# Performance work log

Measured on AMD Instinct MI355X. Metric: run time of the kernel, lower is better.

Reference implementation:

```python
import jax, jax.numpy as jnp
import numpy as np

N = 4096      # tokens
D = 4096      # input_dim
O = 4096      # output_dim
E = 8         # n_experts
R = 16        # LoRA rank (same for all experts)
K = 2         # top_k
TEMP = 1.0    # temperature
ALPHA = 1.0   # LoRA alpha


def setup_inputs() -> dict:
    key = jax.random.key(0)
    ks = jax.random.split(key, 7)
    std = 1.0 / np.sqrt(R)  # LoRALayer init: randn(input_dim, rank) * 1/sqrt(rank)
    return {
        "x": jax.random.normal(ks[0], (N, D), jnp.float32),
        "linear_w": jax.random.normal(ks[1], (D, O), jnp.float32) * 0.02,  # base nn.Linear weight (stored [in,out])
        "linear_b": jnp.zeros((O,), jnp.float32),
        "lora_A": jax.random.normal(ks[2], (E, D, R), jnp.float32) * std,
        "lora_B": jax.random.normal(ks[3], (E, R, O), jnp.float32) * 0.02,  # torch inits B to 0; randomized for nontrivial test
        "gate_w": jax.random.normal(ks[4], (E + 1, D), jnp.float32) * 0.02,  # E+1 GateLayers, each [D,1]
        "bvv": jax.random.randint(ks[5], (N, E), 0, 2, jnp.int32),  # basis_variant_binary_vector (unused in static gating)
    }


def reference(x, linear_w, linear_b, lora_A, lora_B, gate_w, bvv):
    # base path: nn.Linear
    base = x @ linear_w + linear_b                                   # [N, O]
    # all experts evaluated densely: alpha * (x @ A_e @ B_e), batched as grouped GEMMs
    lora = ALPHA * jnp.einsum("ner,ero->neo",
                              jnp.einsum("nd,edr->ner", x, lora_A),
                              lora_B)                                # [N, E, O]
    outputs = jnp.concatenate([base[:, None, :], lora], axis=1)      # [N, E+1, O]

    # static top-k gating
    logits = x @ gate_w.T                                            # [N, E+1]
    base_logits, lora_logits = logits[:, :1], logits[:, 1:]
    top_vals, top_idx = jax.lax.top_k(lora_logits, K)                # [N, K]
    rows = jnp.arange(x.shape[0])[:, None]
    # torch: zeros.scatter(top_idx, top_vals) -> non-selected experts keep logit 0.0
    lora_sparse = jnp.zeros_like(lora_logits).at[rows, top_idx].set(top_vals)
    gates = jax.nn.softmax(
        jnp.concatenate([base_logits, lora_sparse], axis=-1) / TEMP, axis=-1
    )                                                                # [N, E+1]

    return jnp.sum(outputs * gates[..., None], axis=1)               # [N, O]
```

## Files before the change

kernel.cpp:

```cpp
#include <hip/hip_runtime.h>
#include <hip/hip_bf16.h>
#include <math.h>

constexpr int Ncfg = 4096;
constexpr int Dcfg = 4096;
constexpr int Ocfg = 4096;
constexpr int Ecfg = 8;
constexpr int Rcfg = 16;
constexpr int KD   = Dcfg + Ecfg * Rcfg;
constexpr float ALPHA_C = 1.0f;
constexpr double TEMP_C = 1.0;

constexpr size_t BT_OFF = 0;
constexpr size_t AP_OFF = BT_OFF + (size_t)Ocfg * KD * 2;
constexpr size_t AT_OFF = AP_OFF + (size_t)Ncfg * KD * 2;
constexpr size_t G_OFF  = AT_OFF + (size_t)Ecfg * Rcfg * Dcfg * 2;

typedef short bf16x8 __attribute__((ext_vector_type(8)));
typedef float f32x4  __attribute__((ext_vector_type(4)));

__device__ __forceinline__ void async_load16(const __hip_bfloat16* g, __hip_bfloat16* l) {
  __builtin_amdgcn_global_load_lds((__attribute__((address_space(1))) void*)(g),
                                   (__attribute__((address_space(3))) void*)(l), 16, 0, 0);
}

__global__ __launch_bounds__(256) void prep_parallel_kernel(
    const float* __restrict__ x,  const float* __restrict__ gw,
    const float* __restrict__ W,  const float* __restrict__ lB,
    const float* __restrict__ lA,
    float* __restrict__ gates, __hip_bfloat16* __restrict__ Ap,
    __hip_bfloat16* __restrict__ BT, __hip_bfloat16* __restrict__ AT) {
  __shared__ union {
    float tile[64][65];
    float atile[256][17];
  } sm;
  const int bid = blockIdx.x;
  const int tid = threadIdx.x;

  if (bid < 512) {
    const int wave = tid >> 6, lane = tid & 63;
    const int na = bid * 8 + wave * 2, nb = na + 1;
    const float4* xa4 = (const float4*)(x + (size_t)na * Dcfg);
    const float4* xb4 = (const float4*)(x + (size_t)nb * Dcfg);
    const float4* gw4 = (const float4*)gw;
    double accA[9], accB[9];
#pragma unroll
    for (int e = 0; e < 9; e++) { accA[e] = 0.0; accB[e] = 0.0; }
    for (int i = 0; i < 16; i++) {
      int fi = lane + 64 * i;
      float4 xa = xa4[fi], xb = xb4[fi];
#pragma unroll
      for (int e = 0; e < 9; e++) {
        float4 w = gw4[e * 1024 + fi];
        accA[e] += (double)xa.x * (double)w.x + (double)xa.y * (double)w.y +
                   (double)xa.z * (double)w.z + (double)xa.w * (double)w.w;
        accB[e] += (double)xb.x * (double)w.x + (double)xb.y * (double)w.y +
                   (double)xb.z * (double)w.z + (double)xb.w * (double)w.w;
      }
    }
#pragma unroll
    for (int off = 32; off >= 1; off >>= 1) {
#pragma unroll
      for (int e = 0; e < 9; e++) {
        accA[e] += __shfl_xor(accA[e], off, 64);
        accB[e] += __shfl_xor(accB[e], off, 64);
      }
    }
    float g0A_l = 0.f, g0B_l = 0.f;
    if (lane == 0) {
#pragma unroll
      for (int r = 0; r < 2; r++) {
        double lg[9];
#pragma unroll
        for (int e = 0; e < 9; e++) lg[e] = r ? accB[e] : accA[e];
        int i1 = 1;
        for (int e = 2; e <= 8; e++) if (lg[e] > lg[i1]) i1 = e;
        int i2 = -1; double v2 = -1e300;
        for (int e = 1; e <= 8; e++) if (e != i1 && lg[e] > v2) { v2 = lg[e]; i2 = e; }
        double vals[9];
        vals[0] = lg[0];
        for (int e = 1; e <= 8; e++) vals[e] = (e == i1 || e == i2) ? lg[e] : 0.0;
        double mx = vals[0];
        for (int e = 1; e < 9; e++) mx = fmax(mx, vals[e]);
        double se = 0.0, ex[9];
        for (int e = 0; e < 9; e++) { ex[e] = exp((vals[e] - mx) / TEMP_C); se += ex[e]; }
        const int n = r ? nb : na;
        for (int e = 0; e < 9; e++) gates[n * 16 + e] = (float)(ex[e] / se);
        if (r == 0) g0A_l = (float)(ex[0] / se); else g0B_l = (float)(ex[0] / se);
      }
    }
    const float g0A = __shfl(g0A_l, 0, 64);
    const float g0B = __shfl(g0B_l, 0, 64);
    __hip_bfloat16* ara = Ap + (size_t)na * KD;
    __hip_bfloat16* arb = Ap + (size_t)nb * KD;
    for (int i = 0; i < 16; i++) {
      int fi = lane + 64 * i;
      float4 xa = xa4[fi], xb = xb4[fi];
      union { ushort4 u; __hip_bfloat16 h[4]; } p;
      p.h[0] = __float2bfloat16(g0A * xa.x);
      p.h[1] = __float2bfloat16(g0A * xa.y);
      p.h[2] = __float2bfloat16(g0A * xa.z);
      p.h[3] = __float2bfloat16(g0A * xa.w);
      *(ushort4*)(ara + (size_t)fi * 4) = p.u;
      p.h[0] = __float2bfloat16(g0B * xb.x);
      p.h[1] = __float2bfloat16(g0B * xb.y);
      p.h[2] = __float2bfloat16(g0B * xb.z);
      p.h[3] = __float2bfloat16(g0B * xb.w);
      *(ushort4*)(arb + (size_t)fi * 4) = p.u;
    }
  } else if (bid < 4736) {
    const float* src; int r0, c0, dstOff;
    if (bid < 4608) {
      int id = bid - 512;
      src = W; r0 = (id & 63) * 64; c0 = (id >> 6) * 64; dstOff = 0;
    } else {
      int id = bid - 4608;
      src = lB; r0 = (id & 1) * 64; c0 = (id >> 1) * 64; dstOff = Dcfg;
    }
#pragma unroll
    for (int it = 0; it < 4; it++) {
      int flat = it * 256 + tid;
      int i = flat >> 4, f = flat & 15;
      float4 v = *(const float4*)(src + (size_t)(r0 + i) * Ocfg + c0 + 4 * f);
      sm.tile[i][4 * f + 0] = v.x;
      sm.tile[i][4 * f + 1] = v.y;
      sm.tile[i][4 * f + 2] = v.z;
      sm.tile[i][4 * f + 3] = v.w;
    }
    __syncthreads();
#pragma unroll
    for (int it = 0; it < 4; it++) {
      int flat = it * 256 + tid;
      int j = flat >> 4, q = flat & 15;
      union { ushort4 u; __hip_bfloat16 h[4]; } p;
      p.h[0] = __float2bfloat16(sm.tile[4 * q + 0][j]);
      p.h[1] = __float2bfloat16(sm.tile[4 * q + 1][j]);
      p.h[2] = __float2bfloat16(sm.tile[4 * q + 2][j]);
      p.h[3] = __float2bfloat16(sm.tile[4 * q + 3][j]);
      *(ushort4*)(BT + (size_t)(c0 + j) * KD + dstOff + r0 + 4 * q) = p.u;
    }
  } else {
    const int id = bid - 4736;
    const int e = id >> 4, d0 = (id & 15) * 256;
#pragma unroll
    for (int it = 0; it < 16; it++) {
      int idx = it * 256 + tid;
      int d = idx >> 4, rr = idx & 15;
      sm.atile[d][rr] = lA[((size_t)e * Dcfg + d0 + d) * Rcfg + rr];
    }
    __syncthreads();
#pragma unroll
    for (int rr = 0; rr < Rcfg; rr++) {
      AT[((size_t)e * Rcfg + rr) * Dcfg + d0 + tid] = __float2bfloat16(sm.atile[tid][rr]);
    }
  }
}

__global__ __launch_bounds__(512) void lora_t_kernel(
    const float* __restrict__ x, const __hip_bfloat16* __restrict__ AT,
    const float* __restrict__ gates, __hip_bfloat16* __restrict__ Ap) {
  const int n0 = blockIdx.x * 16;
  const int tid = threadIdx.x;
  const int wave = tid >> 6, lane = tid & 63;
  const int m = lane & 15, quad = lane >> 4;
  const int kbase = wave * 512;

  f32x4 acc[8] = {};
  const float* xrow = x + (size_t)(n0 + m) * Dcfg + kbase + quad * 8;
  const __hip_bfloat16* atb = AT + (size_t)m * Dcfg + kbase + quad * 8;
#pragma unroll 2
  for (int kb = 0; kb < 512; kb += 32) {
    float4 x0 = *(const float4*)(xrow + kb);
    float4 x1 = *(const float4*)(xrow + kb + 4);
    union { bf16x8 v; __hip_bfloat16 h[8]; } a;
    a.h[0] = __float2bfloat16(x0.x); a.h[1] = __float2bfloat16(x0.y);
    a.h[2] = __float2bfloat16(x0.z); a.h[3] = __float2bfloat16(x0.w);
    a.h[4] = __float2bfloat16(x1.x); a.h[5] = __float2bfloat16(x1.y);
    a.h[6] = __float2bfloat16(x1.z); a.h[7] = __float2bfloat16(x1.w);
#pragma unroll
    for (int e = 0; e < Ecfg; e++) {
      bf16x8 b = *(const bf16x8*)(atb + (size_t)e * Rcfg * Dcfg + kb);
      acc[e] = __builtin_amdgcn_mfma_f32_16x16x32_bf16(a.v, b, acc[e], 0, 0, 0);
    }
  }
  __shared__ f32x4 red[8][8][64];
#pragma unroll
  for (int e = 0; e < Ecfg; e++) red[wave][e][lane] = acc[e];
  __syncthreads();
  {
    const int e = wave;
    f32x4 s = red[0][e][lane];
#pragma unroll
    for (int w = 1; w < 8; w++) s += red[w][e][lane];
#pragma unroll
    for (int rg = 0; rg < 4; rg++) {
      int nn = n0 + quad * 4 + rg;
      float g = gates[nn * 16 + 1 + e];
      Ap[(size_t)nn * KD + Dcfg + e * Rcfg + m] = __float2bfloat16(ALPHA_C * g * s[rg]);
    }
  }
}

__global__ __launch_bounds__(256) void gemm_kernel(
    const __hip_bfloat16* __restrict__ Ap, const __hip_bfloat16* __restrict__ BT,
    const float* __restrict__ gates, const float* __restrict__ bias,
    float* __restrict__ out) {
  __shared__ __hip_bfloat16 As[128 * 32];
  __shared__ __hip_bfloat16 Bs[128 * 32];
  const int tid = threadIdx.x;
  const int m0 = blockIdx.y * 128, n0 = blockIdx.x * 128;
  const int wave = tid >> 6, lane = tid & 63;
  const int wm = (wave & 1) * 64, wn = (wave >> 1) * 64;
  const int mr = lane & 15, quad = lane >> 4;

  f32x4 acc[4][4] = {};

  const int srow = tid >> 2;
  const int kc = (tid & 3) * 8;
  const __hip_bfloat16* gA0 = Ap + (size_t)(m0 + srow) * KD + kc;
  const __hip_bfloat16* gA1 = gA0 + (size_t)64 * KD;
  const __hip_bfloat16* gB0 = BT + (size_t)(n0 + srow) * KD + kc;
  const __hip_bfloat16* gB1 = gB0 + (size_t)64 * KD;
  __hip_bfloat16* lA0 = As + tid * 8;
  __hip_bfloat16* lA1 = As + 64 * 32 + tid * 8;
  __hip_bfloat16* lB0 = Bs + tid * 8;
  __hip_bfloat16* lB1 = Bs + 64 * 32 + tid * 8;

  for (int kb = 0; kb < KD; kb += 32) {
    __syncthreads();
    async_load16(gA0 + kb, lA0);
    async_load16(gA1 + kb, lA1);
    async_load16(gB0 + kb, lB0);
    async_load16(gB1 + kb, lB1);
    asm volatile("s_waitcnt vmcnt(0)" ::: "memory");
    __syncthreads();

    bf16x8 a[4], b[4];
#pragma unroll
    for (int i = 0; i < 4; i++)
      a[i] = *(const bf16x8*)&As[(wm + i * 16 + mr) * 32 + quad * 8];
#pragma unroll
    for (int j = 0; j < 4; j++)
      b[j] = *(const bf16x8*)&Bs[(wn + j * 16 + mr) * 32 + quad * 8];
#pragma unroll
    for (int i = 0; i < 4; i++)
#pragma unroll
      for (int j = 0; j < 4; j++)
        acc[i][j] = __builtin_amdgcn_mfma_f32_16x16x32_bf16(a[i], b[j], acc[i][j], 0, 0, 0);
  }

#pragma unroll
  for (int i = 0; i < 4; i++) {
    const int rowb = m0 + wm + i * 16 + quad * 4;
#pragma unroll
    for (int rg = 0; rg < 4; rg++) {
      const int row = rowb + rg;
      const float g0 = gates[row * 16];
#pragma unroll
      for (int j = 0; j < 4; j++) {
        const int col = n0 + wn + j * 16 + mr;
        out[(size_t)row * Ocfg + col] = acc[i][j][rg] + g0 * bias[col];
      }
    }
  }
}

extern "C" void kernel_launch(void* const* d_in, const int* in_sizes, int n_in,
                              void* d_out, int out_size, void* d_ws, size_t ws_size,
                              hipStream_t stream) {
  const float* x  = (const float*)d_in[0];
  const float* W  = (const float*)d_in[1];
  const float* b  = (const float*)d_in[2];
  const float* lA = (const float*)d_in[3];
  const float* lB = (const float*)d_in[4];
  const float* gw = (const float*)d_in[5];
  float* out = (float*)d_out;

  char* ws = (char*)d_ws;
  __hip_bfloat16* BT    = (__hip_bfloat16*)(ws + BT_OFF);
  __hip_bfloat16* Ap    = (__hip_bfloat16*)(ws + AP_OFF);
  __hip_bfloat16* AT    = (__hip_bfloat16*)(ws + AT_OFF);
  float*          gates = (float*)(ws + G_OFF);

  prep_parallel_kernel<<<dim3(4864), 256, 0, stream>>>(x, gw, W, lB, lA, gates, Ap, BT, AT);
  lora_t_kernel<<<dim3(Ncfg / 16), 512, 0, stream>>>(x, AT, gates, Ap);
  gemm_kernel<<<dim3(Ocfg / 128, Ncfg / 128), 256, 0, stream>>>(Ap, BT, gates, b, out);
}
```

Before: 400.9 us.

## Rewrite GEMM with 256x256 tiles, double-buffered async LDS loads, and swizzling

Replaces the 128x128 single-buffered GEMM with a 256x256 tile, 512-thread kernel that double-buffers K=64 tiles in 128KB of LDS, loading the next tile while MFMAs run, and XOR-swizzles the LDS layout to avoid bank conflicts. The work is split into four MFMA phases interleaved with barriers and s_setprio. This targets the load-then-wait stall in the old loop and raises data reuse per tile. The larger tile gives only 256 blocks, so CU occupancy and load balance may suffer, and the large LDS footprint limits resident blocks.

```diff
diff --git a/kernel.cpp b/kernel.cpp
--- a/kernel.cpp
+++ b/kernel.cpp
@@ -8,6 +8,7 @@
 constexpr int Ecfg = 8;
 constexpr int Rcfg = 16;
 constexpr int KD   = Dcfg + Ecfg * Rcfg;
+constexpr int NKT  = KD / 64;
 constexpr float ALPHA_C = 1.0f;
 constexpr double TEMP_C = 1.0;
 
@@ -201,66 +202,152 @@
   }
 }
 
-__global__ __launch_bounds__(256) void gemm_kernel(
+#define STG(gbase, lbase, u, ktile)                                              \
+  __builtin_amdgcn_global_load_lds(                                              \
+      (__attribute__((address_space(1))) void*)((gbase) + (size_t)(u) * 64 * KD  \
+                                                + (size_t)(ktile) * 64),         \
+      (__attribute__((address_space(3))) void*)((lbase) + (u) * 8192 + dst),     \
+      16, 0, 0)
+
+__global__ __launch_bounds__(512, 2) void gemm_kernel(
     const __hip_bfloat16* __restrict__ Ap, const __hip_bfloat16* __restrict__ BT,
     const float* __restrict__ gates, const float* __restrict__ bias,
     float* __restrict__ out) {
-  __shared__ __hip_bfloat16 As[128 * 32];
-  __shared__ __hip_bfloat16 Bs[128 * 32];
+  __shared__ char smem[131072];
   const int tid = threadIdx.x;
-  const int m0 = blockIdx.y * 128, n0 = blockIdx.x * 128;
+  const int m0 = blockIdx.y * 256, n0 = blockIdx.x * 256;
   const int wave = tid >> 6, lane = tid & 63;
-  const int wm = (wave & 1) * 64, wn = (wave >> 1) * 64;
+  const int wm = wave >> 2, wn = wave & 3;
   const int mr = lane & 15, quad = lane >> 4;
 
-  f32x4 acc[4][4] = {};
-
-  const int srow = tid >> 2;
-  const int kc = (tid & 3) * 8;
-  const __hip_bfloat16* gA0 = Ap + (size_t)(m0 + srow) * KD + kc;
-  const __hip_bfloat16* gA1 = gA0 + (size_t)64 * KD;
-  const __hip_bfloat16* gB0 = BT + (size_t)(n0 + srow) * KD + kc;
-  const __hip_bfloat16* gB1 = gB0 + (size_t)64 * KD;
-  __hip_bfloat16* lA0 = As + tid * 8;
-  __hip_bfloat16* lA1 = As + 64 * 32 + tid * 8;
-  __hip_bfloat16* lB0 = Bs + tid * 8;
-  __hip_bfloat16* lB1 = Bs + 64 * 32 + tid * 8;
-
-  for (int kb = 0; kb < KD; kb += 32) {
-    __syncthreads();
-    async_load16(gA0 + kb, lA0);
-    async_load16(gA1 + kb, lA1);
-    async_load16(gB0 + kb, lB0);
-    async_load16(gB1 + kb, lB1);
-    asm volatile("s_waitcnt vmcnt(0)" ::: "memory");
-    __syncthreads();
-
-    bf16x8 a[4], b[4];
-#pragma unroll
-    for (int i = 0; i < 4; i++)
-      a[i] = *(const bf16x8*)&As[(wm + i * 16 + mr) * 32 + quad * 8];
-#pragma unroll
-    for (int j = 0; j < 4; j++)
-      b[j] = *(const bf16x8*)&Bs[(wn + j * 16 + mr) * 32 + quad * 8];
-#pragma unroll
-    for (int i = 0; i < 4; i++)
-#pragma unroll
-      for (int j = 0; j < 4; j++)
-        acc[i][j] = __builtin_amdgcn_mfma_f32_16x16x32_bf16(a[i], b[j], acc[i][j], 0, 0, 0);
-  }
-
-#pragma unroll
-  for (int i = 0; i < 4; i++) {
-    const int rowb = m0 + wm + i * 16 + quad * 4;
-#pragma unroll
-    for (int rg = 0; rg < 4; rg++) {
+  const int trow = tid >> 3;
+  const int cswz = ((tid & 7) << 3) ^ (((tid >> 5) & 1) << 4);
+  const __hip_bfloat16* gA = Ap + (size_t)(m0 + trow) * KD + cswz;
+  const __hip_bfloat16* gB = BT + (size_t)(n0 + trow) * KD + cswz;
+  const int dst = tid << 4;
+
+  const int swz  = (quad << 4) ^ ((mr & 4) << 3);
+  const int aoff = (wm * 128 + mr) * 128 + swz;
+  const int boff = (wn * 64 + mr) * 128 + swz;
+
+  f32x4 acc[8][4] = {};
+
+  STG(gA, smem,          0, 0); STG(gA, smem,          1, 0);
+  STG(gA, smem,          2, 0); STG(gA, smem,          3, 0);
+  STG(gB, smem + 32768,  0, 0); STG(gB, smem + 32768,  1, 0);
+  STG(gB, smem + 32768,  2, 0); STG(gB, smem + 32768,  3, 0);
+  STG(gA, smem + 65536,  0, 1); STG(gA, smem + 65536,  1, 1);
+  STG(gA, smem + 65536,  2, 1); STG(gA, smem + 65536,  3, 1);
+  STG(gB, smem + 98304,  0, 1); STG(gB, smem + 98304,  1, 1);
+  asm volatile("s_waitcnt vmcnt(6)" ::: "memory");
+  __builtin_amdgcn_s_barrier();
+
+  for (int kt = 0; kt < NKT; ++kt) {
+    const bool odd = kt & 1;
+    const char* At = odd ? (smem + 65536) : smem;
+    const char* Bt = odd ? (smem + 98304) : (smem + 32768);
+    char* An = odd ? smem : (smem + 65536);
+    char* Bn = odd ? (smem + 32768) : (smem + 98304);
+
+    bf16x8 a[4][2], b0r[2][2], b1r[2][2];
+
+#pragma unroll
+    for (int i = 0; i < 4; ++i)
+#pragma unroll
+      for (int kh = 0; kh < 2; ++kh)
+        a[i][kh] = *(const bf16x8*)(At + aoff + i * 2048 + kh * 64);
+#pragma unroll
+    for (int j = 0; j < 2; ++j)
+#pragma unroll
+      for (int kh = 0; kh < 2; ++kh)
+        b0r[j][kh] = *(const bf16x8*)(Bt + boff + j * 2048 + kh * 64);
+    if (kt + 1 < NKT) { STG(gB, Bn, 2, kt + 1); STG(gB, Bn, 3, kt + 1); }
+    __builtin_amdgcn_s_barrier();
+    asm volatile("s_waitcnt lgkmcnt(0)" ::: "memory");
+    __builtin_amdgcn_s_setprio(1);
+#pragma unroll
+    for (int i = 0; i < 4; ++i)
+#pragma unroll
+      for (int j = 0; j < 2; ++j)
+#pragma unroll
+        for (int kh = 0; kh < 2; ++kh)
+          acc[i][j] = __builtin_amdgcn_mfma_f32_16x16x32_bf16(a[i][kh], b0r[j][kh], acc[i][j], 0, 0, 0);
+    __builtin_amdgcn_s_setprio(0);
+    __builtin_amdgcn_s_barrier();
+
+#pragma unroll
+    for (int j = 0; j < 2; ++j)
+#pragma unroll
+      for (int kh = 0; kh < 2; ++kh)
+        b1r[j][kh] = *(const bf16x8*)(Bt + boff + (2 + j) * 2048 + kh * 64);
+    __builtin_amdgcn_s_barrier();
+    asm volatile("s_waitcnt lgkmcnt(0)" ::: "memory");
+    __builtin_amdgcn_s_setprio(1);
+#pragma unroll
+    for (int i = 0; i < 4; ++i)
+#pragma unroll
+      for (int j = 0; j < 2; ++j)
+#pragma unroll
+        for (int kh = 0; kh < 2; ++kh)
+          acc[i][2 + j] = __builtin_amdgcn_mfma_f32_16x16x32_bf16(a[i][kh], b1r[j][kh], acc[i][2 + j], 0, 0, 0);
+    __builtin_amdgcn_s_setprio(0);
+    __builtin_amdgcn_s_barrier();
+
+#pragma unroll
+    for (int i = 0; i < 4; ++i)
+#pragma unroll
+      for (int kh = 0; kh < 2; ++kh)
+        a[i][kh] = *(const bf16x8*)(At + aoff + (4 + i) * 2048 + kh * 64);
+    __builtin_amdgcn_s_barrier();
+    asm volatile("s_waitcnt lgkmcnt(0)" ::: "memory");
+    __builtin_amdgcn_s_setprio(1);
+#pragma unroll
+    for (int i = 0; i < 4; ++i)
+#pragma unroll
+      for (int j = 0; j < 2; ++j)
+#pragma unroll
+        for (int kh = 0; kh < 2; ++kh)
+          acc[4 + i][2 + j] = __builtin_amdgcn_mfma_f32_16x16x32_bf16(a[i][kh], b1r[j][kh], acc[4 + i][2 + j], 0, 0, 0);
+    __builtin_amdgcn_s_setprio(0);
+    __builtin_amdgcn_s_barrier();
+
+    if (kt + 2 < NKT) {
+      char* Ac = (char*)At; char* Bc = (char*)Bt;
+      STG(gA, Ac, 0, kt + 2); STG(gA, Ac, 1, kt + 2);
+      STG(gA, Ac, 2, kt + 2); STG(gA, Ac, 3, kt + 2);
+      STG(gB, Bc, 0, kt + 2); STG(gB, Bc, 1, kt + 2);
+    }
+    __builtin_amdgcn_s_setprio(1);
+#pragma unroll
+    for (int i = 0; i < 4; ++i)
+#pragma unroll
+      for (int j = 0; j < 2; ++j)
+#pragma unroll
+        for (int kh = 0; kh < 2; ++kh)
+          acc[4 + i][j] = __builtin_amdgcn_mfma_f32_16x16x32_bf16(a[i][kh], b0r[j][kh], acc[4 + i][j], 0, 0, 0);
+    __builtin_amdgcn_s_setprio(0);
+    if (kt + 2 < NKT) {
+      asm volatile("s_waitcnt vmcnt(6)" ::: "memory");
+    } else if (kt + 1 < NKT) {
+      asm volatile("s_waitcnt vmcnt(0)" ::: "memory");
+    }
+    if (kt + 1 < NKT) __builtin_amdgcn_s_barrier();
+  }
+
+  float bv[4];
+#pragma unroll
+  for (int j = 0; j < 4; ++j) bv[j] = bias[n0 + wn * 64 + j * 16 + mr];
+#pragma unroll
+  for (int i = 0; i < 8; ++i) {
+    const int rowb = m0 + wm * 128 + i * 16 + quad * 4;
+#pragma unroll
+    for (int rg = 0; rg < 4; ++rg) {
       const int row = rowb + rg;
       const float g0 = gates[row * 16];
-#pragma unroll
-      for (int j = 0; j < 4; j++) {
-        const int col = n0 + wn + j * 16 + mr;
-        out[(size_t)row * Ocfg + col] = acc[i][j][rg] + g0 * bias[col];
-      }
+      float* orow = out + (size_t)row * Ocfg + n0 + wn * 64 + mr;
+#pragma unroll
+      for (int j = 0; j < 4; ++j)
+        orow[j * 16] = acc[i][j][rg] + g0 * bv[j];
     }
   }
 }
@@ -284,5 +371,5 @@
 
   prep_parallel_kernel<<<dim3(4864), 256, 0, stream>>>(x, gw, W, lB, lA, gates, Ap, BT, AT);
   lora_t_kernel<<<dim3(Ncfg / 16), 512, 0, stream>>>(x, AT, gates, Ap);
-  gemm_kernel<<<dim3(Ocfg / 128, Ncfg / 128), 256, 0, stream>>>(Ap, BT, gates, b, out);
-}
+  gemm_kernel<<<dim3(Ocfg / 256, Ncfg / 256), 512, 0, stream>>>(Ap, BT, gates, b, out);
+}
```

Result: faster. 359.2 us (-10.4%).
